# Optimization experiments

Measured on AMD Instinct MI355X. Metric: run time of the kernel, lower is better.

## Reference

```python
import jax, jax.numpy as jnp
import numpy as np


def setup_inputs() -> dict:
    key = jax.random.key(0)
    k1, k2 = jax.random.split(key)
    N, C, T, K = 8192, 3, 2048, 10
    Xt = jax.random.normal(k1, (N, C, T), dtype=jnp.float32)
    y_true = jax.random.randint(k2, (N,), 0, K, dtype=jnp.int64)
    return {"Xt": Xt, "y_true": y_true, "num_classes": K}


def reference(Xt, y_true, num_classes):
    # Within-Class Sum of Squares: for each class k,
    #   loss_k = mean((Xk - mean(Xk, axis=0))**2)  (mean over all elements)
    # total = mean over classes. Assumes all num_classes labels are present
    # (matches torch.unique iteration under this data distribution).
    N = Xt.shape[0]
    D = Xt.shape[1] * Xt.shape[2]  # elements per sample
    sums = jax.ops.segment_sum(Xt, y_true, num_segments=num_classes)        # [K, C, T]
    counts = jax.ops.segment_sum(jnp.ones((N,), Xt.dtype), y_true,
                                 num_segments=num_classes)                  # [K]
    means = sums / counts[:, None, None]                                    # [K, C, T]
    sq = jnp.square(Xt - means[y_true])                                     # [N, C, T]
    sq_per_sample = sq.reshape(N, -1).sum(axis=1)                           # [N]
    sq_sums = jax.ops.segment_sum(sq_per_sample, y_true,
                                  num_segments=num_classes)                 # [K]
    per_class_mse = sq_sums / (counts * D)                                  # [K]
    return per_class_mse.mean()
```

## Files before the change

### kernel.cpp

```cpp
#include <hip/hip_runtime.h>

#define N_SAMP 8192
#define D_DIM 6144
#define K_CLS 10
#define CHUNK 32
#define NWIN (N_SAMP / CHUNK)
#define COLS_PER_BLOCK 1024
#define NGROUPS (D_DIM / COLS_PER_BLOCK)
#define NBLK (NGROUPS * NWIN)

typedef float f4 __attribute__((ext_vector_type(4)));

__device__ __forceinline__ void atom_add_dev(float* p, float v) {
    __hip_atomic_fetch_add(p, v, __ATOMIC_RELAXED, __HIP_MEMORY_SCOPE_AGENT);
}
__device__ __forceinline__ float load_dev(const float* p) {
    return __hip_atomic_load(p, __ATOMIC_RELAXED, __HIP_MEMORY_SCOPE_AGENT);
}
__device__ __forceinline__ float wave_sum(float x) {
#pragma unroll
    for (int o = 32; o > 0; o >>= 1) x += __shfl_down(x, o, 64);
    return x;
}

__global__ __launch_bounds__(1024) void build_sort(const int* __restrict__ y,
                                                   int* __restrict__ counts,
                                                   int* __restrict__ sorted,
                                                   float* __restrict__ S1,
                                                   float* __restrict__ s2sum,
                                                   unsigned* __restrict__ ctr) {
    __shared__ int M[K_CLS * 1024];
    __shared__ int wsum[16];
    const int tid = threadIdx.x;
    const int lane = tid & 63;
    const int wid = tid >> 6;

    {
        f4 z = {0.f, 0.f, 0.f, 0.f};
        f4* p = (f4*)S1;
#pragma unroll
        for (int i = 0; i < (K_CLS * D_DIM) / (4 * 1024); ++i)
            p[i * 1024 + tid] = z;
        if (tid < K_CLS) s2sum[tid] = 0.f;
        if (tid == K_CLS) *ctr = 0u;
    }

    const int base = tid * 8;
    const int4 ya = ((const int4*)y)[tid * 2];
    const int4 yb = ((const int4*)y)[tid * 2 + 1];
    int yy[8] = {ya.x, ya.y, ya.z, ya.w, yb.x, yb.y, yb.z, yb.w};
    int h[K_CLS];
#pragma unroll
    for (int k = 0; k < K_CLS; ++k) h[k] = 0;
#pragma unroll
    for (int i = 0; i < 8; ++i)
#pragma unroll
        for (int k = 0; k < K_CLS; ++k) h[k] += (yy[i] == k) ? 1 : 0;
#pragma unroll
    for (int k = 0; k < K_CLS; ++k) M[k * 1024 + tid] = h[k];
    __syncthreads();

    int loc[K_CLS];
    int run = 0;
#pragma unroll
    for (int j = 0; j < K_CLS; ++j) { loc[j] = run; run += M[tid * K_CLS + j]; }
    int v = run;
#pragma unroll
    for (int d = 1; d < 64; d <<= 1) {
        int n = __shfl_up(v, d, 64);
        if (lane >= d) v += n;
    }
    if (lane == 63) wsum[wid] = v;
    __syncthreads();
    int wbase = 0;
#pragma unroll
    for (int w = 0; w < 16; ++w) wbase += (w < wid) ? wsum[w] : 0;
    const int tbase = wbase + (v - run);
    __syncthreads();
#pragma unroll
    for (int j = 0; j < K_CLS; ++j) M[tid * K_CLS + j] = tbase + loc[j];
    __syncthreads();

    if (tid < K_CLS) {
        const int s = M[tid * 1024];
        const int e = (tid == K_CLS - 1) ? N_SAMP : M[(tid + 1) * 1024];
        counts[tid] = e - s;
    }

    int off[K_CLS];
#pragma unroll
    for (int k = 0; k < K_CLS; ++k) off[k] = M[k * 1024 + tid];
#pragma unroll
    for (int i = 0; i < 8; ++i)
#pragma unroll
        for (int k = 0; k < K_CLS; ++k)
            if (yy[i] == k) sorted[off[k]++] = (k << 16) | (base + i);
}

__global__ __launch_bounds__(256, 6) void wcss_accum(const float* __restrict__ X,
                                                     const int* __restrict__ sorted,
                                                     const int* __restrict__ counts,
                                                     float* __restrict__ S1,
                                                     float* __restrict__ s2sum,
                                                     unsigned* __restrict__ ctr,
                                                     float* __restrict__ out) {
    __shared__ float wred[4];
    __shared__ int last_s;
    const int tid = threadIdx.x;
    const int lane = tid & 63;
    const int wid = tid >> 6;
    const int col0 = blockIdx.x * COLS_PER_BLOCK + tid * 4;

    const int* wp = sorted + blockIdx.y * CHUNK;
    int w[CHUNK];
#pragma unroll
    for (int r = 0; r < CHUNK; ++r)
        w[r] = __builtin_amdgcn_readfirstlane(wp[r]);

    const char* xb = (const char*)X + (size_t)col0 * 4;
#define LOADR(r) (*(const f4*)(xb + \
        (size_t)(unsigned)((w[(r)] & 0xffff) * (D_DIM * 4))))

    f4 a1 = {0.f, 0.f, 0.f, 0.f};
    float s2c = 0.f;
    int kcur = w[0] >> 16;

    f4 qa0, qa1, qa2, qa3, qb0, qb1, qb2, qb3, qc0, qc1, qc2, qc3;

#define ISSUE(Q, b) { Q##0 = LOADR(4*(b)+0); Q##1 = LOADR(4*(b)+1); \
                      Q##2 = LOADR(4*(b)+2); Q##3 = LOADR(4*(b)+3); }
#define PIN(Q) asm volatile("" :: "v"(Q##0), "v"(Q##1), "v"(Q##2), "v"(Q##3) \
                            : "memory")
#define EAT1(r, V) { \
        const int yk = w[(r)] >> 16; \
        if (yk != kcur) {  \
            float* p1 = S1 + kcur * D_DIM + col0; \
            atom_add_dev(p1 + 0, a1.x); atom_add_dev(p1 + 1, a1.y); \
            atom_add_dev(p1 + 2, a1.z); atom_add_dev(p1 + 3, a1.w); \
            float r_ = wave_sum(s2c); \
            if (lane == 0) atom_add_dev(&s2sum[kcur], r_); \
            a1 = (f4){0.f, 0.f, 0.f, 0.f}; s2c = 0.f; kcur = yk; } \
        a1 += V; \
        s2c += V.x * V.x + V.y * V.y + V.z * V.z + V.w * V.w; }
#define EAT4(b, Q) { EAT1(4*(b)+0, Q##0) EAT1(4*(b)+1, Q##1) \
                     EAT1(4*(b)+2, Q##2) EAT1(4*(b)+3, Q##3) }

    ISSUE(qa, 0) ISSUE(qb, 1) ISSUE(qc, 2)
    PIN(qa); EAT4(0, qa) ISSUE(qa, 3)
    PIN(qb); EAT4(1, qb) ISSUE(qb, 4)
    PIN(qc); EAT4(2, qc) ISSUE(qc, 5)
    PIN(qa); EAT4(3, qa) ISSUE(qa, 6)
    PIN(qb); EAT4(4, qb) ISSUE(qb, 7)
    PIN(qc); EAT4(5, qc)
    PIN(qa); EAT4(6, qa)
    PIN(qb); EAT4(7, qb)
#undef EAT4
#undef EAT1
#undef PIN
#undef ISSUE
#undef LOADR

    float* p1 = S1 + kcur * D_DIM + col0;
    atom_add_dev(p1 + 0, a1.x); atom_add_dev(p1 + 1, a1.y);
    atom_add_dev(p1 + 2, a1.z); atom_add_dev(p1 + 3, a1.w);
    float rw = wave_sum(s2c);
    if (lane == 0) atom_add_dev(&s2sum[kcur], rw);

    asm volatile("s_waitcnt vmcnt(0)" ::: "memory");
    __syncthreads();
    if (tid == 0) {
        unsigned t = __hip_atomic_fetch_add(ctr, 1u, __ATOMIC_RELAXED,
                                            __HIP_MEMORY_SCOPE_AGENT);
        last_s = (t == (unsigned)(NBLK - 1)) ? 1 : 0;
    }
    __syncthreads();
    if (!last_s) return;

    float part = 0.f;
#pragma unroll
    for (int k = 0; k < K_CLS; ++k) {
        const float c = (float)counts[k];
        const float inv2 = 1.0f / (c * c * (float)D_DIM * (float)K_CLS);
        const float* Sk = S1 + k * D_DIM;
        for (int j = 0; j < D_DIM / 256; ++j) {
            float vv = load_dev(&Sk[j * 256 + tid]);
            part -= vv * vv * inv2;
        }
        if (tid == 0)
            part += load_dev(&s2sum[k]) / (c * (float)D_DIM * (float)K_CLS);
    }
    float r = wave_sum(part);
    if (lane == 0) wred[wid] = r;
    __syncthreads();
    if (tid == 0) *out = wred[0] + wred[1] + wred[2] + wred[3];
}

extern "C" void kernel_launch(void* const* d_in, const int* in_sizes, int n_in,
                              void* d_out, int out_size, void* d_ws, size_t ws_size,
                              hipStream_t stream) {
    const float* X = (const float*)d_in[0];
    const int* y = (const int*)d_in[1];

    float* S1 = (float*)d_ws;
    float* s2sum = S1 + K_CLS * D_DIM;
    int* counts = (int*)(s2sum + K_CLS);
    int* sorted = counts + K_CLS;
    unsigned* ctr = (unsigned*)(sorted + N_SAMP);
    float* out = (float*)d_out;

    build_sort<<<dim3(1), dim3(1024), 0, stream>>>(y, counts, sorted,
                                                   S1, s2sum, ctr);
    wcss_accum<<<dim3(NGROUPS, NWIN), dim3(256), 0, stream>>>(X, sorted, counts,
                                                              S1, s2sum, ctr, out);
}
```

Measured before the change: 332.6 us.

## Use wider row windows with precomputed class boundaries and single-wave blocks

Each block now covers 256 sorted rows instead of 32 and a 256-column slice with a single 64-thread wave, which cuts the number of atomic flushes into the per-class sums. The sort kernel precomputes per-window class boundary metadata, so the accumulation loop runs at most two segments and drops the per-row class check. Row offsets are staged through LDS and read with readfirstlane, and loads are batched eight at a time. The larger grid of single-wave blocks changes occupancy and latency hiding, and one block now streams 256 rows with less software pipelining than before.

```diff
diff --git a/kernel.cpp b/kernel.cpp
--- a/kernel.cpp
+++ b/kernel.cpp
@@ -3,11 +3,11 @@
 #define N_SAMP 8192
 #define D_DIM 6144
 #define K_CLS 10
-#define CHUNK 32
-#define NWIN (N_SAMP / CHUNK)
-#define COLS_PER_BLOCK 1024
-#define NGROUPS (D_DIM / COLS_PER_BLOCK)
-#define NBLK (NGROUPS * NWIN)
+#define RWIN 256
+#define NWIN2 (N_SAMP / RWIN)
+#define CG 24
+#define TPB 64
+#define NBLK (CG * NWIN2)
 
 typedef float f4 __attribute__((ext_vector_type(4)));
 
@@ -28,9 +28,11 @@
                                                    int* __restrict__ sorted,
                                                    float* __restrict__ S1,
                                                    float* __restrict__ s2sum,
-                                                   unsigned* __restrict__ ctr) {
+                                                   unsigned* __restrict__ ctr,
+                                                   int4* __restrict__ win_meta) {
     __shared__ int M[K_CLS * 1024];
     __shared__ int wsum[16];
+    __shared__ int cls_start[K_CLS + 1];
     const int tid = threadIdx.x;
     const int lane = tid & 63;
     const int wid = tid >> 6;
@@ -85,6 +87,21 @@
         const int s = M[tid * 1024];
         const int e = (tid == K_CLS - 1) ? N_SAMP : M[(tid + 1) * 1024];
         counts[tid] = e - s;
+        cls_start[tid] = s;
+        if (tid == 0) cls_start[K_CLS] = N_SAMP;
+    }
+    __syncthreads();
+
+    if (tid < NWIN2) {
+        const int lo = tid * RWIN, hi = lo + RWIN;
+        int kA = 0;
+#pragma unroll
+        for (int k = 0; k < K_CLS; ++k)
+            if (cls_start[k] <= lo) kA = k;
+        const int bnd = cls_start[kA + 1];
+        const int bpos = (bnd < hi) ? (bnd - lo) : RWIN;
+        const int kB = (bpos < RWIN) ? (kA + 1) : kA;
+        win_meta[tid] = make_int4(bpos, kA, kB, 0);
     }
 
     int off[K_CLS];
@@ -97,84 +114,75 @@
             if (yy[i] == k) sorted[off[k]++] = (k << 16) | (base + i);
 }
 
-__global__ __launch_bounds__(256, 6) void wcss_accum(const float* __restrict__ X,
-                                                     const int* __restrict__ sorted,
-                                                     const int* __restrict__ counts,
-                                                     float* __restrict__ S1,
-                                                     float* __restrict__ s2sum,
-                                                     unsigned* __restrict__ ctr,
-                                                     float* __restrict__ out) {
-    __shared__ float wred[4];
-    __shared__ int last_s;
+__global__ __launch_bounds__(TPB) void wcss_accum(const float* __restrict__ X,
+                                                  const int* __restrict__ sorted,
+                                                  const int4* __restrict__ win_meta,
+                                                  const int* __restrict__ counts,
+                                                  float* __restrict__ S1,
+                                                  float* __restrict__ s2sum,
+                                                  unsigned* __restrict__ ctr,
+                                                  float* __restrict__ out) {
+    __shared__ int off_lds[RWIN];
     const int tid = threadIdx.x;
-    const int lane = tid & 63;
-    const int wid = tid >> 6;
-    const int col0 = blockIdx.x * COLS_PER_BLOCK + tid * 4;
-
-    const int* wp = sorted + blockIdx.y * CHUNK;
-    int w[CHUNK];
-#pragma unroll
-    for (int r = 0; r < CHUNK; ++r)
-        w[r] = __builtin_amdgcn_readfirstlane(wp[r]);
+    const int wy = blockIdx.y;
+    const int col0 = blockIdx.x * (TPB * 4) + tid * 4;
+
+    {
+        const int4 pp = ((const int4*)(sorted + wy * RWIN))[tid];
+        off_lds[tid * 4 + 0] = (pp.x & 0xffff) * (D_DIM * 4);
+        off_lds[tid * 4 + 1] = (pp.y & 0xffff) * (D_DIM * 4);
+        off_lds[tid * 4 + 2] = (pp.z & 0xffff) * (D_DIM * 4);
+        off_lds[tid * 4 + 3] = (pp.w & 0xffff) * (D_DIM * 4);
+    }
+    __syncthreads();
+
+    const int4 meta = win_meta[wy];
+    const int bpos = __builtin_amdgcn_readfirstlane(meta.x);
+    const int kA   = __builtin_amdgcn_readfirstlane(meta.y);
+    const int kB   = __builtin_amdgcn_readfirstlane(meta.z);
 
     const char* xb = (const char*)X + (size_t)col0 * 4;
-#define LOADR(r) (*(const f4*)(xb + \
-        (size_t)(unsigned)((w[(r)] & 0xffff) * (D_DIM * 4))))
-
-    f4 a1 = {0.f, 0.f, 0.f, 0.f};
-    float s2c = 0.f;
-    int kcur = w[0] >> 16;
-
-    f4 qa0, qa1, qa2, qa3, qb0, qb1, qb2, qb3, qc0, qc1, qc2, qc3;
-
-#define ISSUE(Q, b) { Q##0 = LOADR(4*(b)+0); Q##1 = LOADR(4*(b)+1); \
-                      Q##2 = LOADR(4*(b)+2); Q##3 = LOADR(4*(b)+3); }
-#define PIN(Q) asm volatile("" :: "v"(Q##0), "v"(Q##1), "v"(Q##2), "v"(Q##3) \
-                            : "memory")
-#define EAT1(r, V) { \
-        const int yk = w[(r)] >> 16; \
-        if (yk != kcur) {  \
-            float* p1 = S1 + kcur * D_DIM + col0; \
-            atom_add_dev(p1 + 0, a1.x); atom_add_dev(p1 + 1, a1.y); \
-            atom_add_dev(p1 + 2, a1.z); atom_add_dev(p1 + 3, a1.w); \
-            float r_ = wave_sum(s2c); \
-            if (lane == 0) atom_add_dev(&s2sum[kcur], r_); \
-            a1 = (f4){0.f, 0.f, 0.f, 0.f}; s2c = 0.f; kcur = yk; } \
-        a1 += V; \
-        s2c += V.x * V.x + V.y * V.y + V.z * V.z + V.w * V.w; }
-#define EAT4(b, Q) { EAT1(4*(b)+0, Q##0) EAT1(4*(b)+1, Q##1) \
-                     EAT1(4*(b)+2, Q##2) EAT1(4*(b)+3, Q##3) }
-
-    ISSUE(qa, 0) ISSUE(qb, 1) ISSUE(qc, 2)
-    PIN(qa); EAT4(0, qa) ISSUE(qa, 3)
-    PIN(qb); EAT4(1, qb) ISSUE(qb, 4)
-    PIN(qc); EAT4(2, qc) ISSUE(qc, 5)
-    PIN(qa); EAT4(3, qa) ISSUE(qa, 6)
-    PIN(qb); EAT4(4, qb) ISSUE(qb, 7)
-    PIN(qc); EAT4(5, qc)
-    PIN(qa); EAT4(6, qa)
-    PIN(qb); EAT4(7, qb)
-#undef EAT4
-#undef EAT1
-#undef PIN
-#undef ISSUE
+
+#define LOADR(r) (*(const f4*)(xb + (size_t)(unsigned) \
+        __builtin_amdgcn_readfirstlane(off_lds[(r)])))
+#define CONSUME(V) { a1 += (V); \
+        s2c += (V).x*(V).x + (V).y*(V).y + (V).z*(V).z + (V).w*(V).w; }
+
+    f4 a1; float s2c; int r;
+#define SEG(sBeg, sEnd, KC)                                                  \
+    {                                                                        \
+        a1 = (f4){0.f, 0.f, 0.f, 0.f}; s2c = 0.f;                            \
+        r = (sBeg);                                                          \
+        for (; r + 8 <= (sEnd); r += 8) {        \
+            f4 v0 = LOADR(r+0), v1 = LOADR(r+1), v2 = LOADR(r+2),            \
+               v3 = LOADR(r+3), v4 = LOADR(r+4), v5 = LOADR(r+5),            \
+               v6 = LOADR(r+6), v7 = LOADR(r+7);                             \
+            asm volatile("" :: "v"(v0), "v"(v1), "v"(v2), "v"(v3),           \
+                               "v"(v4), "v"(v5), "v"(v6), "v"(v7));          \
+            CONSUME(v0) CONSUME(v1) CONSUME(v2) CONSUME(v3)                  \
+            CONSUME(v4) CONSUME(v5) CONSUME(v6) CONSUME(v7)                  \
+        }                                                                    \
+        for (; r < (sEnd); ++r) { f4 vv = LOADR(r); CONSUME(vv) }            \
+        float* p1 = S1 + (KC) * D_DIM + col0;                                \
+        atom_add_dev(p1 + 0, a1.x); atom_add_dev(p1 + 1, a1.y);              \
+        atom_add_dev(p1 + 2, a1.z); atom_add_dev(p1 + 3, a1.w);              \
+        float rs_ = wave_sum(s2c);                                           \
+        if (tid == 0) atom_add_dev(&s2sum[(KC)], rs_);                       \
+    }
+
+    SEG(0, bpos, kA)
+    if (bpos < RWIN) { SEG(bpos, RWIN, kB) }
+#undef SEG
+#undef CONSUME
 #undef LOADR
 
-    float* p1 = S1 + kcur * D_DIM + col0;
-    atom_add_dev(p1 + 0, a1.x); atom_add_dev(p1 + 1, a1.y);
-    atom_add_dev(p1 + 2, a1.z); atom_add_dev(p1 + 3, a1.w);
-    float rw = wave_sum(s2c);
-    if (lane == 0) atom_add_dev(&s2sum[kcur], rw);
-
     asm volatile("s_waitcnt vmcnt(0)" ::: "memory");
-    __syncthreads();
-    if (tid == 0) {
-        unsigned t = __hip_atomic_fetch_add(ctr, 1u, __ATOMIC_RELAXED,
-                                            __HIP_MEMORY_SCOPE_AGENT);
-        last_s = (t == (unsigned)(NBLK - 1)) ? 1 : 0;
-    }
-    __syncthreads();
-    if (!last_s) return;
+    unsigned t = 0;
+    if (tid == 0)
+        t = __hip_atomic_fetch_add(ctr, 1u, __ATOMIC_RELAXED,
+                                   __HIP_MEMORY_SCOPE_AGENT);
+    t = __shfl((int)t, 0, 64);
+    if (t != (unsigned)(NBLK - 1)) return;
 
     float part = 0.f;
 #pragma unroll
@@ -182,17 +190,15 @@
         const float c = (float)counts[k];
         const float inv2 = 1.0f / (c * c * (float)D_DIM * (float)K_CLS);
         const float* Sk = S1 + k * D_DIM;
-        for (int j = 0; j < D_DIM / 256; ++j) {
-            float vv = load_dev(&Sk[j * 256 + tid]);
+        for (int j = 0; j < D_DIM / TPB; ++j) {
+            float vv = load_dev(&Sk[j * TPB + tid]);
             part -= vv * vv * inv2;
         }
         if (tid == 0)
             part += load_dev(&s2sum[k]) / (c * (float)D_DIM * (float)K_CLS);
     }
-    float r = wave_sum(part);
-    if (lane == 0) wred[wid] = r;
-    __syncthreads();
-    if (tid == 0) *out = wred[0] + wred[1] + wred[2] + wred[3];
+    float rr = wave_sum(part);
+    if (tid == 0) *out = rr;
 }
 
 extern "C" void kernel_launch(void* const* d_in, const int* in_sizes, int n_in,
@@ -204,12 +210,16 @@
     float* S1 = (float*)d_ws;
     float* s2sum = S1 + K_CLS * D_DIM;
     int* counts = (int*)(s2sum + K_CLS);
-    int* sorted = counts + K_CLS;
-    unsigned* ctr = (unsigned*)(sorted + N_SAMP);
+    unsigned* ctr = (unsigned*)(counts + K_CLS);
+    char* p = (char*)(ctr + 1);
+    p += (16 - ((uintptr_t)p & 15)) & 15;
+    int4* win_meta = (int4*)p;
+    int* sorted = (int*)(win_meta + NWIN2);
     float* out = (float*)d_out;
 
     build_sort<<<dim3(1), dim3(1024), 0, stream>>>(y, counts, sorted,
-                                                   S1, s2sum, ctr);
-    wcss_accum<<<dim3(NGROUPS, NWIN), dim3(256), 0, stream>>>(X, sorted, counts,
-                                                              S1, s2sum, ctr, out);
-}
+                                                   S1, s2sum, ctr, win_meta);
+    wcss_accum<<<dim3(CG, NWIN2), dim3(TPB), 0, stream>>>(X, sorted, win_meta,
+                                                          counts, S1, s2sum,
+                                                          ctr, out);
+}
```

After: 324.3 us. 1.03x faster.
